# Optimization experiments

Hardware: AMD Instinct MI355X
Metric: run time of the kernel (lower is better)

Reference implementation:

```python
import math
import jax, jax.numpy as jnp
import numpy as np

D, NH, NL, NP = 256, 8, 3, 4
HD = D // NH
SHAPES = np.array([[92, 92], [46, 46], [23, 23]], dtype=np.int32)
LSI = np.concatenate([[0], np.cumsum(SHAPES[:, 0] * SHAPES[:, 1])[:-1]]).astype(np.int32)
LV = int((SHAPES[:, 0] * SHAPES[:, 1]).sum())  # 11109
B, LQ = 2, LV


def setup_inputs() -> dict:
    key = jax.random.key(0)
    ks = jax.random.split(key, 8)
    query = jax.random.normal(ks[0], (B, LQ, D), jnp.float32)
    reference_points = jax.random.uniform(ks[1], (B, LQ, NL, 2), dtype=jnp.float32)
    value_flat = jax.random.normal(ks[2], (B, LV, D), jnp.float32)
    # sampling_offsets: small random weight + structured directional bias (as in _reset_parameters)
    W_off = jax.random.normal(ks[3], (D, NH * NL * NP * 2), jnp.float32) * 0.01
    thetas = np.arange(NH, dtype=np.float64) * (2.0 * math.pi / NH)
    g = np.stack([np.cos(thetas), np.sin(thetas)], axis=-1)
    g = g / np.abs(g).max(axis=-1, keepdims=True)
    g = np.tile(g[:, None, None, :], (1, NL, NP, 1))
    g = g * (np.arange(NP) + 1)[None, None, :, None]
    b_off = jnp.asarray(g.reshape(-1), jnp.float32)
    W_attn = jax.random.normal(ks[4], (D, NH * NL * NP), jnp.float32) * 0.01
    b_attn = jnp.zeros((NH * NL * NP,), jnp.float32)
    W_val = jax.random.normal(ks[5], (D, D), jnp.float32) * (1.0 / math.sqrt(D))
    b_val = jnp.zeros((D,), jnp.float32)
    W_out = jax.random.normal(ks[6], (D, D), jnp.float32) * (1.0 / math.sqrt(D))
    b_out = jnp.zeros((D,), jnp.float32)
    return dict(query=query, reference_points=reference_points, value_flat=value_flat,
                W_val=W_val, b_val=b_val, W_off=W_off, b_off=b_off,
                W_attn=W_attn, b_attn=b_attn, W_out=W_out, b_out=b_out,
                spatial_shapes=jnp.asarray(SHAPES), level_start_index=jnp.asarray(LSI))


def _bilinear_sample(val_l, grid):
    """torch.F.grid_sample(mode='bilinear', padding_mode='zeros', align_corners=False).
    val_l: [B,H,W,nH,hd]; grid: [B,Q,nH,P,2] with (x,y) in [-1,1].
    Returns [B,nH,Q,P,hd]."""
    Bq, H, W, nH, hd = val_l.shape
    Q, P = grid.shape[1], grid.shape[3]
    x = ((grid[..., 0] + 1.0) * W - 1.0) * 0.5   # pixel coords, align_corners=False
    y = ((grid[..., 1] + 1.0) * H - 1.0) * 0.5
    x0f, y0f = jnp.floor(x), jnp.floor(y)
    lx, ly = x - x0f, y - y0f
    x0, y0 = x0f.astype(jnp.int32), y0f.astype(jnp.int32)
    val_bh = val_l.transpose(0, 3, 1, 2, 4).reshape(Bq * nH, H * W, hd)

    def corner(yi, xi, w):
        valid = (xi >= 0) & (xi < W) & (yi >= 0) & (yi < H)
        idx = jnp.clip(yi, 0, H - 1) * W + jnp.clip(xi, 0, W - 1)   # [B,Q,nH,P]
        idx_bh = idx.transpose(0, 2, 1, 3).reshape(Bq * nH, Q * P)
        g = jnp.take_along_axis(val_bh, idx_bh[:, :, None], axis=1)  # [B*nH, Q*P, hd]
        wm = (w * valid.astype(w.dtype)).transpose(0, 2, 1, 3).reshape(Bq * nH, Q * P, 1)
        return g * wm

    out = (corner(y0, x0, (1 - ly) * (1 - lx)) + corner(y0, x0 + 1, (1 - ly) * lx)
           + corner(y0 + 1, x0, ly * (1 - lx)) + corner(y0 + 1, x0 + 1, ly * lx))
    return out.reshape(Bq, nH, Q, P, hd)


def reference(query, reference_points, value_flat, W_val, b_val, W_off, b_off,
              W_attn, b_attn, W_out, b_out, spatial_shapes, level_start_index):
    shapes = np.asarray(spatial_shapes)          # static level geometry
    starts = np.asarray(level_start_index)
    Bq, Lq, _ = query.shape
    value = (value_flat @ W_val + b_val).reshape(Bq, -1, NH, HD)
    off = (query @ W_off + b_off).reshape(Bq, Lq, NH, NL, NP, 2)        # (dy,dx) pixels
    aw = jax.nn.softmax((query @ W_attn + b_attn).reshape(Bq, Lq, NH, NL * NP), axis=-1)
    aw = aw.reshape(Bq, Lq, NH, NL, NP)
    sh_f = jnp.asarray(shapes, jnp.float32)                              # [L,2] = (H,W)
    norm_off = off / sh_f[None, None, None, :, None, :]
    loc = reference_points[:, :, None, :, None, :] + norm_off           # [B,Lq,NH,NL,NP,2] (y,x)
    grid = 2.0 * loc[..., ::-1] - 1.0                                    # (x,y) in [-1,1]
    out = jnp.zeros((Bq, Lq, NH, HD), query.dtype)
    for l in range(NL):
        H, W = int(shapes[l, 0]), int(shapes[l, 1])
        s = int(starts[l])
        val_l = value[:, s:s + H * W].reshape(Bq, H, W, NH, HD)
        sampled = _bilinear_sample(val_l, grid[:, :, :, l])              # [B,NH,Lq,NP,HD]
        out = out + jnp.einsum('bhqpc,bqhp->bqhc', sampled, aw[:, :, :, l])
    return out.reshape(Bq, Lq, D) @ W_out + b_out
```

## Files before the change

### kernel.cpp

```cpp
#include <hip/hip_runtime.h>

#define LQn   11109
#define MTOT  22218

typedef __attribute__((ext_vector_type(8))) short short8;
typedef __attribute__((ext_vector_type(4))) float f32x4;

__device__ __forceinline__ unsigned short f2bf(float f) {
  union { float f; unsigned int u; } v; v.f = f;
  unsigned int r = v.u + 0x7fffu + ((v.u >> 16) & 1u);
  return (unsigned short)(r >> 16);
}

__device__ __forceinline__ int xcd_swz(int bid, int nwg) {
  const int xcd = bid & 7, pos = bid >> 3;
  const int q = nwg >> 3, r = nwg & 7;
  return (xcd < r ? xcd * (q + 1) : r * (q + 1) + (xcd - r) * q) + pos;
}

__global__ __launch_bounds__(256) void prep_weights(
    const float* __restrict__ Wval, const float* __restrict__ Woff,
    const float* __restrict__ Wattn, const float* __restrict__ Wout,
    const float* __restrict__ boff, const float* __restrict__ battn,
    unsigned short* __restrict__ Wval_t, unsigned short* __restrict__ Wcat_t,
    unsigned short* __restrict__ Wout_t, float* __restrict__ bcat) {
  int i = blockIdx.x * 256 + threadIdx.x;
  int n = i >> 8, k = i & 255;
  if (n < 256) {
    Wval_t[i] = f2bf(Wval[k * 256 + n]);
    Wout_t[i] = f2bf(Wout[k * 256 + n]);
  }
  float src = (n < 192) ? Woff[k * 192 + n] : Wattn[k * 96 + (n - 192)];
  Wcat_t[i] = f2bf(src);
  if (i < 288) bcat[i] = (i < 192) ? boff[i] : battn[i - 192];
}

__global__ __launch_bounds__(256) void gemm_fused12(
    const float* __restrict__ Aval,
    const float* __restrict__ Aq,
    const unsigned short* __restrict__ Bval,
    const unsigned short* __restrict__ Bcat,
    const float* __restrict__ bval, const float* __restrict__ bcat,
    unsigned short* __restrict__ value16,
    float* __restrict__ logits) {
  __shared__ unsigned short As[64][40];
  __shared__ unsigned short Bs[64][40];

  const int bm = blockIdx.x;
  int bn = blockIdx.y;
  const bool is2 = bn >= 4;
  if (is2) bn -= 4;
  const float* __restrict__ A = is2 ? Aq : Aval;
  const unsigned short* __restrict__ Bt = is2 ? Bcat : Bval;
  const float* __restrict__ bias = is2 ? bcat : bval;
  const int N = is2 ? 288 : 256;

  const int t = threadIdx.x;
  const int wave = t >> 6, lane = t & 63;
  const int wm = wave >> 1, wn = wave & 1;
  const int quad = lane >> 4, l16 = lane & 15;

  const int ldr = t >> 2;
  const int ldk = (t & 3) * 8;
  const int arow = bm * 64 + ldr;
  const int brow = bn * 64 + ldr;
  const bool aok = arow < MTOT;
  const bool bok = brow < N;
  const float* ap = A + (size_t)arow * 256 + ldk;
  const unsigned short* bp = Bt + (size_t)brow * 256 + ldk;

  f32x4 acc[2][2];
  for (int i = 0; i < 2; i++)
    for (int j = 0; j < 2; j++) acc[i][j] = (f32x4){0.f, 0.f, 0.f, 0.f};

  float4 a0c = {0.f,0.f,0.f,0.f}, a1c = a0c, a0n = a0c, a1n = a0c;
  uint4 bvc = {0u,0u,0u,0u}, bvn = bvc;
  if (aok) { a0c = *(const float4*)(ap);      a1c = *(const float4*)(ap + 4);
             a0n = *(const float4*)(ap + 32); a1n = *(const float4*)(ap + 36); }
  if (bok) { bvc = *(const uint4*)(bp);       bvn = *(const uint4*)(bp + 32); }

#pragma unroll
  for (int kb = 0; kb < 8; kb++) {
    ushort4 lo, hi;
    lo.x = f2bf(a0c.x); lo.y = f2bf(a0c.y); lo.z = f2bf(a0c.z); lo.w = f2bf(a0c.w);
    hi.x = f2bf(a1c.x); hi.y = f2bf(a1c.y); hi.z = f2bf(a1c.z); hi.w = f2bf(a1c.w);
    __syncthreads();
    *(ushort4*)(&As[ldr][ldk]) = lo;
    *(ushort4*)(&As[ldr][ldk + 4]) = hi;
    *(uint4*)(&Bs[ldr][ldk]) = bvc;
    __syncthreads();
    a0c = a0n; a1c = a1n; bvc = bvn;
    if (kb < 6) {
      const int k2 = (kb + 2) * 32;
      if (aok) { a0n = *(const float4*)(ap + k2); a1n = *(const float4*)(ap + k2 + 4); }
      if (bok) bvn = *(const uint4*)(bp + k2);
    }
    short8 af[2], bfr[2];
    for (int i = 0; i < 2; i++)
      af[i] = *(const short8*)(&As[wm * 32 + i * 16 + l16][quad * 8]);
    for (int j = 0; j < 2; j++)
      bfr[j] = *(const short8*)(&Bs[wn * 32 + j * 16 + l16][quad * 8]);
    for (int i = 0; i < 2; i++)
      for (int j = 0; j < 2; j++)
        acc[i][j] = __builtin_amdgcn_mfma_f32_16x16x32_bf16(af[i], bfr[j], acc[i][j], 0, 0, 0);
  }

  for (int i = 0; i < 2; i++)
    for (int j = 0; j < 2; j++) {
      int colg = bn * 64 + wn * 32 + j * 16 + l16;
      if (colg >= N) continue;
      float bsv = bias[colg];
      int row0 = bm * 64 + wm * 32 + i * 16 + quad * 4;
      for (int r = 0; r < 4; r++) {
        int rg = row0 + r;
        if (rg >= MTOT) continue;
        float v = acc[i][j][r] + bsv;
        if (is2) logits[(size_t)rg * 288 + colg] = v;
        else     value16[(size_t)rg * 256 + colg] = f2bf(v);
      }
    }
}

__global__ __launch_bounds__(256) void gemm_a16(
    const unsigned short* __restrict__ A,
    const unsigned short* __restrict__ Bt,
    const float* __restrict__ bias,
    float* __restrict__ C) {
  __shared__ unsigned short As[64][40];
  __shared__ unsigned short Bs[64][40];

  const int t = threadIdx.x;
  const int bm = blockIdx.x, bn = blockIdx.y;
  const int wave = t >> 6, lane = t & 63;
  const int wm = wave >> 1, wn = wave & 1;
  const int quad = lane >> 4, l16 = lane & 15;

  const int ldr = t >> 2;
  const int ldk = (t & 3) * 8;
  const int arow = bm * 64 + ldr;
  const int brow = bn * 64 + ldr;
  const bool aok = arow < MTOT;
  const unsigned short* ap = A + (size_t)arow * 256 + ldk;
  const unsigned short* bp = Bt + (size_t)brow * 256 + ldk;

  f32x4 acc[2][2];
  for (int i = 0; i < 2; i++)
    for (int j = 0; j < 2; j++) acc[i][j] = (f32x4){0.f, 0.f, 0.f, 0.f};

  uint4 avc = {0u,0u,0u,0u}, avn = avc, bvc, bvn;
  if (aok) { avc = *(const uint4*)(ap); avn = *(const uint4*)(ap + 32); }
  bvc = *(const uint4*)(bp);
  bvn = *(const uint4*)(bp + 32);

#pragma unroll
  for (int kb = 0; kb < 8; kb++) {
    __syncthreads();
    *(uint4*)(&As[ldr][ldk]) = avc;
    *(uint4*)(&Bs[ldr][ldk]) = bvc;
    __syncthreads();
    avc = avn; bvc = bvn;
    if (kb < 6) {
      const int k2 = (kb + 2) * 32;
      if (aok) avn = *(const uint4*)(ap + k2);
      bvn = *(const uint4*)(bp + k2);
    }
    short8 af[2], bfr[2];
    for (int i = 0; i < 2; i++)
      af[i] = *(const short8*)(&As[wm * 32 + i * 16 + l16][quad * 8]);
    for (int j = 0; j < 2; j++)
      bfr[j] = *(const short8*)(&Bs[wn * 32 + j * 16 + l16][quad * 8]);
    for (int i = 0; i < 2; i++)
      for (int j = 0; j < 2; j++)
        acc[i][j] = __builtin_amdgcn_mfma_f32_16x16x32_bf16(af[i], bfr[j], acc[i][j], 0, 0, 0);
  }

  for (int i = 0; i < 2; i++)
    for (int j = 0; j < 2; j++) {
      int colg = bn * 64 + wn * 32 + j * 16 + l16;
      float bsv = bias[colg];
      int row0 = bm * 64 + wm * 32 + i * 16 + quad * 4;
      for (int r = 0; r < 4; r++) {
        int rg = row0 + r;
        if (rg < MTOT)
          __builtin_nontemporal_store(acc[i][j][r] + bsv, &C[(size_t)rg * 256 + colg]);
      }
    }
}

__global__ __launch_bounds__(256) void msda_sample4(
    const unsigned short* __restrict__ value16,
    const float* __restrict__ logits,
    const float* __restrict__ refp,
    unsigned short* __restrict__ sampled) {
  __shared__ float          tw[8][96][4];
  __shared__ unsigned short ti[8][96][4];
  __shared__ float hmx[8][8], hrd[8][8];
  __shared__ float rfs[8][6];

  const int t = threadIdx.x;
  const int nbid = xcd_swz(blockIdx.x, gridDim.x);
  const int qbase = nbid * 8;

  if (t < 48) {
    int q = t / 6;
    if (qbase + q < MTOT) rfs[q][t - q * 6] = refp[(size_t)qbase * 6 + t];
  }
  if (t >= 64 && t < 128) {
    int tt = t - 64;
    int q = tt >> 3, h = tt & 7;
    int bq = qbase + q;
    if (bq < MTOT) {
      const float* lrow = logits + (size_t)bq * 288 + 192 + h * 12;
      float mx = -1e30f;
#pragma unroll
      for (int i = 0; i < 12; i++) mx = fmaxf(mx, lrow[i]);
      float den = 0.f;
#pragma unroll
      for (int i = 0; i < 12; i++) den += __expf(lrow[i] - mx);
      hmx[q][h] = mx;
      hrd[q][h] = 1.0f / den;
    }
  }
  __syncthreads();

  {
    const int Hs[3] = {92, 46, 23};
    const int Ss[3] = {0, 8464, 10580};
#pragma unroll
    for (int r = 0; r < 3; r++) {
      const int task = t + r * 256;
      const int q = task / 96, s = task - q * 96;
      const int bq = qbase + q;
      if (bq < MTOT) {
        const int h = s / 12, pl = s - h * 12;
        const int l = pl >> 2;
        const int H = Hs[l], W = Hs[l], S = Ss[l];
        const float* lrow = logits + (size_t)bq * 288;
        const float aw = __expf(lrow[192 + s] - hmx[q][h]) * hrd[q][h];
        const float offy = lrow[2 * s], offx = lrow[2 * s + 1];
        const float x = rfs[q][l * 2 + 1] * W + offx - 0.5f;
        const float y = rfs[q][l * 2 + 0] * H + offy - 0.5f;
        const float xf = floorf(x), yf = floorf(y);
        const int x0 = (int)xf, y0 = (int)yf;
        const float lx = x - xf, ly = y - yf;
        const bool xv0 = (x0 >= 0) & (x0 < W), xv1 = (x0 + 1 >= 0) & (x0 + 1 < W);
        const bool yv0 = (y0 >= 0) & (y0 < H), yv1 = (y0 + 1 >= 0) & (y0 + 1 < H);
        const int xc0 = min(max(x0, 0), W - 1), xc1 = min(max(x0 + 1, 0), W - 1);
        const int yc0 = min(max(y0, 0), H - 1), yc1 = min(max(y0 + 1, 0), H - 1);
        const int slot = pl * 8 + h;
        ti[q][slot][0] = (unsigned short)(S + yc0 * W + xc0);
        ti[q][slot][1] = (unsigned short)(S + yc0 * W + xc1);
        ti[q][slot][2] = (unsigned short)(S + yc1 * W + xc0);
        ti[q][slot][3] = (unsigned short)(S + yc1 * W + xc1);
        tw[q][slot][0] = (yv0 & xv0) ? aw * (1.f - ly) * (1.f - lx) : 0.f;
        tw[q][slot][1] = (yv0 & xv1) ? aw * (1.f - ly) * lx : 0.f;
        tw[q][slot][2] = (yv1 & xv0) ? aw * ly * (1.f - lx) : 0.f;
        tw[q][slot][3] = (yv1 & xv1) ? aw * ly * lx : 0.f;
      }
    }
  }
  __syncthreads();

  {
    const int w = t >> 6, lane = t & 63;
    const int q = w * 2 + (lane >> 5);
    const int h = (lane >> 2) & 7, cg = lane & 3;
    const int bq = qbase + q;
    const bool qv = bq < MTOT;
    const int bqc = qv ? bq : 0;
    const char* __restrict__ vb =
        (const char*)value16 + (size_t)(bqc / LQn) * ((size_t)LQn * 512);
    const unsigned laneoff = (unsigned)h * 64u + (unsigned)cg * 16u;

    float a0 = 0.f, a1 = 0.f, a2 = 0.f, a3 = 0.f;
    float a4 = 0.f, a5 = 0.f, a6 = 0.f, a7 = 0.f;
#pragma unroll
    for (int p = 0; p < 12; p++) {
      const int slot = p * 8 + h;
      const ushort4 tiv = *(const ushort4*)(&ti[q][slot][0]);
      const f32x4 wv = *(const f32x4*)(&tw[q][slot][0]);
#pragma unroll
      for (int k = 0; k < 4; k++) {
        const unsigned pix =
            (k == 0) ? tiv.x : (k == 1) ? tiv.y : (k == 2) ? tiv.z : tiv.w;
        const float wgt = wv[k];
        const uint4 u = *(const uint4*)(vb + ((pix << 9) + laneoff));
        a0 += wgt * __uint_as_float(u.x << 16);
        a1 += wgt * __uint_as_float(u.x & 0xffff0000u);
        a2 += wgt * __uint_as_float(u.y << 16);
        a3 += wgt * __uint_as_float(u.y & 0xffff0000u);
        a4 += wgt * __uint_as_float(u.z << 16);
        a5 += wgt * __uint_as_float(u.z & 0xffff0000u);
        a6 += wgt * __uint_as_float(u.w << 16);
        a7 += wgt * __uint_as_float(u.w & 0xffff0000u);
      }
    }
    if (qv) {
      uint4 o;
      o.x = (unsigned)f2bf(a0) | ((unsigned)f2bf(a1) << 16);
      o.y = (unsigned)f2bf(a2) | ((unsigned)f2bf(a3) << 16);
      o.z = (unsigned)f2bf(a4) | ((unsigned)f2bf(a5) << 16);
      o.w = (unsigned)f2bf(a6) | ((unsigned)f2bf(a7) << 16);
      *(uint4*)(sampled + (size_t)bq * 256 + h * 32 + cg * 8) = o;
    }
  }
}

extern "C" void kernel_launch(void* const* d_in, const int* in_sizes, int n_in,
                              void* d_out, int out_size, void* d_ws, size_t ws_size,
                              hipStream_t stream) {
  const float* query      = (const float*)d_in[0];
  const float* refp       = (const float*)d_in[1];
  const float* value_flat = (const float*)d_in[2];
  const float* W_val      = (const float*)d_in[3];
  const float* b_val      = (const float*)d_in[4];
  const float* W_off      = (const float*)d_in[5];
  const float* b_off      = (const float*)d_in[6];
  const float* W_attn     = (const float*)d_in[7];
  const float* b_attn     = (const float*)d_in[8];
  const float* W_out      = (const float*)d_in[9];
  const float* b_out      = (const float*)d_in[10];

  char* w = (char*)d_ws;
  size_t o = 0;
  auto carve = [&](size_t bytes) -> void* {
    void* p = (void*)(w + o);
    o += (bytes + 255) & ~(size_t)255;
    return p;
  };
  unsigned short* Wval_t  = (unsigned short*)carve(256 * 256 * 2);
  unsigned short* Wcat_t  = (unsigned short*)carve(288 * 256 * 2);
  unsigned short* Wout_t  = (unsigned short*)carve(256 * 256 * 2);
  float*          bcat    = (float*)carve(288 * 4);
  unsigned short* value16 = (unsigned short*)carve((size_t)MTOT * 256 * 2);
  float*          logits  = (float*)carve((size_t)MTOT * 288 * 4);
  unsigned short* samp_bf = (unsigned short*)carve((size_t)MTOT * 256 * 2);

  prep_weights<<<288, 256, 0, stream>>>(W_val, W_off, W_attn, W_out, b_off, b_attn,
                                        Wval_t, Wcat_t, Wout_t, bcat);

  const int mg = (MTOT + 63) / 64;
  dim3 g12(mg, 9);
  gemm_fused12<<<g12, 256, 0, stream>>>(value_flat, query, Wval_t, Wcat_t,
                                        b_val, bcat, value16, logits);

  const int sgrid = (MTOT + 7) / 8;
  msda_sample4<<<sgrid, 256, 0, stream>>>(value16, logits, refp, samp_bf);

  dim3 g3(mg, 4);
  gemm_a16<<<g3, 256, 0, stream>>>(samp_bf, Wout_t, b_out, (float*)d_out);
}
```

Before: 190.5 us.

## Double-buffer LDS in GEMMs and store value in head-major layout

Both GEMM kernels now use two LDS buffers so the next K-slice is written while the current one feeds MFMA, which cuts the loop from two barriers per step to one. The value projection output is rewritten as [batch][head][pixel][32], and the sampler's addressing is changed to match, so gathers for one head fall in a compact per-head region. This aims to improve cache locality of the bilinear gathers and reduce GEMM synchronisation stalls, at the cost of doubled LDS and scattered 2-byte stores in the GEMM epilogue.

```diff
diff --git a/kernel.cpp b/kernel.cpp
--- a/kernel.cpp
+++ b/kernel.cpp
@@ -43,8 +43,8 @@
     const float* __restrict__ bval, const float* __restrict__ bcat,
     unsigned short* __restrict__ value16,
     float* __restrict__ logits) {
-  __shared__ unsigned short As[64][40];
-  __shared__ unsigned short Bs[64][40];
+  __shared__ unsigned short As[2][64][40];
+  __shared__ unsigned short Bs[2][64][40];
 
   const int bm = blockIdx.x;
   int bn = blockIdx.y;
@@ -79,30 +79,41 @@
              a0n = *(const float4*)(ap + 32); a1n = *(const float4*)(ap + 36); }
   if (bok) { bvc = *(const uint4*)(bp);       bvn = *(const uint4*)(bp + 32); }
 
-#pragma unroll
-  for (int kb = 0; kb < 8; kb++) {
+  {
     ushort4 lo, hi;
     lo.x = f2bf(a0c.x); lo.y = f2bf(a0c.y); lo.z = f2bf(a0c.z); lo.w = f2bf(a0c.w);
     hi.x = f2bf(a1c.x); hi.y = f2bf(a1c.y); hi.z = f2bf(a1c.z); hi.w = f2bf(a1c.w);
-    __syncthreads();
-    *(ushort4*)(&As[ldr][ldk]) = lo;
-    *(ushort4*)(&As[ldr][ldk + 4]) = hi;
-    *(uint4*)(&Bs[ldr][ldk]) = bvc;
-    __syncthreads();
-    a0c = a0n; a1c = a1n; bvc = bvn;
-    if (kb < 6) {
-      const int k2 = (kb + 2) * 32;
-      if (aok) { a0n = *(const float4*)(ap + k2); a1n = *(const float4*)(ap + k2 + 4); }
-      if (bok) bvn = *(const uint4*)(bp + k2);
+    *(ushort4*)(&As[0][ldr][ldk]) = lo;
+    *(ushort4*)(&As[0][ldr][ldk + 4]) = hi;
+    *(uint4*)(&Bs[0][ldr][ldk]) = bvc;
+  }
+  __syncthreads();
+
+#pragma unroll
+  for (int kb = 0; kb < 8; kb++) {
+    const int cur = kb & 1;
+    if (kb < 7) {
+      ushort4 lo, hi;
+      lo.x = f2bf(a0n.x); lo.y = f2bf(a0n.y); lo.z = f2bf(a0n.z); lo.w = f2bf(a0n.w);
+      hi.x = f2bf(a1n.x); hi.y = f2bf(a1n.y); hi.z = f2bf(a1n.z); hi.w = f2bf(a1n.w);
+      *(ushort4*)(&As[cur ^ 1][ldr][ldk]) = lo;
+      *(ushort4*)(&As[cur ^ 1][ldr][ldk + 4]) = hi;
+      *(uint4*)(&Bs[cur ^ 1][ldr][ldk]) = bvn;
+      if (kb < 6) {
+        const int k2 = (kb + 2) * 32;
+        if (aok) { a0n = *(const float4*)(ap + k2); a1n = *(const float4*)(ap + k2 + 4); }
+        if (bok) bvn = *(const uint4*)(bp + k2);
+      }
     }
     short8 af[2], bfr[2];
     for (int i = 0; i < 2; i++)
-      af[i] = *(const short8*)(&As[wm * 32 + i * 16 + l16][quad * 8]);
+      af[i] = *(const short8*)(&As[cur][wm * 32 + i * 16 + l16][quad * 8]);
     for (int j = 0; j < 2; j++)
-      bfr[j] = *(const short8*)(&Bs[wn * 32 + j * 16 + l16][quad * 8]);
+      bfr[j] = *(const short8*)(&Bs[cur][wn * 32 + j * 16 + l16][quad * 8]);
     for (int i = 0; i < 2; i++)
       for (int j = 0; j < 2; j++)
         acc[i][j] = __builtin_amdgcn_mfma_f32_16x16x32_bf16(af[i], bfr[j], acc[i][j], 0, 0, 0);
+    __syncthreads();
   }
 
   for (int i = 0; i < 2; i++)
@@ -115,8 +126,13 @@
         int rg = row0 + r;
         if (rg >= MTOT) continue;
         float v = acc[i][j][r] + bsv;
-        if (is2) logits[(size_t)rg * 288 + colg] = v;
-        else     value16[(size_t)rg * 256 + colg] = f2bf(v);
+        if (is2) {
+          logits[(size_t)rg * 288 + colg] = v;
+        } else {
+          int b = (rg >= LQn) ? 1 : 0;
+          int p = rg - b * LQn;
+          value16[((size_t)(b * 8 + (colg >> 5)) * LQn + p) * 32 + (colg & 31)] = f2bf(v);
+        }
       }
     }
 }
@@ -126,8 +142,8 @@
     const unsigned short* __restrict__ Bt,
     const float* __restrict__ bias,
     float* __restrict__ C) {
-  __shared__ unsigned short As[64][40];
-  __shared__ unsigned short Bs[64][40];
+  __shared__ unsigned short As[2][64][40];
+  __shared__ unsigned short Bs[2][64][40];
 
   const int t = threadIdx.x;
   const int bm = blockIdx.x, bn = blockIdx.y;
@@ -152,26 +168,31 @@
   bvc = *(const uint4*)(bp);
   bvn = *(const uint4*)(bp + 32);
 
+  *(uint4*)(&As[0][ldr][ldk]) = avc;
+  *(uint4*)(&Bs[0][ldr][ldk]) = bvc;
+  __syncthreads();
+
 #pragma unroll
   for (int kb = 0; kb < 8; kb++) {
-    __syncthreads();
-    *(uint4*)(&As[ldr][ldk]) = avc;
-    *(uint4*)(&Bs[ldr][ldk]) = bvc;
-    __syncthreads();
-    avc = avn; bvc = bvn;
-    if (kb < 6) {
-      const int k2 = (kb + 2) * 32;
-      if (aok) avn = *(const uint4*)(ap + k2);
-      bvn = *(const uint4*)(bp + k2);
+    const int cur = kb & 1;
+    if (kb < 7) {
+      *(uint4*)(&As[cur ^ 1][ldr][ldk]) = avn;
+      *(uint4*)(&Bs[cur ^ 1][ldr][ldk]) = bvn;
+      if (kb < 6) {
+        const int k2 = (kb + 2) * 32;
+        if (aok) avn = *(const uint4*)(ap + k2);
+        bvn = *(const uint4*)(bp + k2);
+      }
     }
     short8 af[2], bfr[2];
     for (int i = 0; i < 2; i++)
-      af[i] = *(const short8*)(&As[wm * 32 + i * 16 + l16][quad * 8]);
+      af[i] = *(const short8*)(&As[cur][wm * 32 + i * 16 + l16][quad * 8]);
     for (int j = 0; j < 2; j++)
-      bfr[j] = *(const short8*)(&Bs[wn * 32 + j * 16 + l16][quad * 8]);
+      bfr[j] = *(const short8*)(&Bs[cur][wn * 32 + j * 16 + l16][quad * 8]);
     for (int i = 0; i < 2; i++)
       for (int j = 0; j < 2; j++)
         acc[i][j] = __builtin_amdgcn_mfma_f32_16x16x32_bf16(af[i], bfr[j], acc[i][j], 0, 0, 0);
+    __syncthreads();
   }
 
   for (int i = 0; i < 2; i++)
@@ -270,7 +291,7 @@
     const int bqc = qv ? bq : 0;
     const char* __restrict__ vb =
         (const char*)value16 + (size_t)(bqc / LQn) * ((size_t)LQn * 512);
-    const unsigned laneoff = (unsigned)h * 64u + (unsigned)cg * 16u;
+    const unsigned laneoff = (unsigned)h * (LQn * 64u) + (unsigned)cg * 16u;
 
     float a0 = 0.f, a1 = 0.f, a2 = 0.f, a3 = 0.f;
     float a4 = 0.f, a5 = 0.f, a6 = 0.f, a7 = 0.f;
@@ -284,7 +305,7 @@
         const unsigned pix =
             (k == 0) ? tiv.x : (k == 1) ? tiv.y : (k == 2) ? tiv.z : tiv.w;
         const float wgt = wv[k];
-        const uint4 u = *(const uint4*)(vb + ((pix << 9) + laneoff));
+        const uint4 u = *(const uint4*)(vb + ((pix << 6) + laneoff));
         a0 += wgt * __uint_as_float(u.x << 16);
         a1 += wgt * __uint_as_float(u.x & 0xffff0000u);
         a2 += wgt * __uint_as_float(u.y << 16);
```

New measurement: 187.0 us. About the same (-1.9%).
